# Performance work log

Measured on AMD Instinct MI355X. Metric: run time of the kernel, lower is better.

The kernel has to match this reference:

```python
import math
import jax, jax.numpy as jnp
import numpy as np

B, T, D = 128, 243, 1024   # batch, motion frames, latent_dim
N, L = 77, 512             # text tokens, text_latent_dim
H = 16                     # num_head -> head_dim 64
EPS = 1e-5


def _ln(x, g, b):
    m = x.mean(-1, keepdims=True)
    v = jnp.var(x, axis=-1, keepdims=True)
    return (x - m) * jax.lax.rsqrt(v + EPS) * g + b


def setup_inputs() -> dict:
    key = jax.random.key(0)
    ks = jax.random.split(key, 16)
    s = 0.02
    return {
        "x": jax.random.normal(ks[0], (B, T, D), jnp.float32),
        "xf": jax.random.normal(ks[1], (B, N, L), jnp.float32),
        "emb": jax.random.normal(ks[2], (B, T, D), jnp.float32),
        "ln_g": jnp.ones((D,), jnp.float32), "ln_b": jnp.zeros((D,), jnp.float32),
        "tln_g": jnp.ones((L,), jnp.float32), "tln_b": jnp.zeros((L,), jnp.float32),
        "Wq": jax.random.normal(ks[3], (D, D), jnp.float32) * s,
        "bq": jnp.zeros((D,), jnp.float32),
        "Wk": jax.random.normal(ks[4], (L, D), jnp.float32) * s,
        "bk": jnp.zeros((D,), jnp.float32),
        "Wv": jax.random.normal(ks[5], (L, D), jnp.float32) * s,
        "bv": jnp.zeros((D,), jnp.float32),
        "We": jax.random.normal(ks[6], (D, 2 * D), jnp.float32) * s,  # emb_layers Linear(time_embed_dim=D, 2D)
        "be": jnp.zeros((2 * D,), jnp.float32),
        "ln2_g": jnp.ones((D,), jnp.float32), "ln2_b": jnp.zeros((D,), jnp.float32),
        "Wo": jax.random.normal(ks[7], (D, D), jnp.float32) * s,     # zero_module in torch; random here for non-trivial baseline
        "bo": jnp.zeros((D,), jnp.float32),
    }


def reference(x, xf, emb, ln_g, ln_b, tln_g, tln_b, Wq, bq, Wk, bk, Wv, bv,
              We, be, ln2_g, ln2_b, Wo, bo):
    B_, T_, D_ = x.shape
    dh = D_ // H
    # cross-attention: queries from motion tokens, keys/values from text
    q = (_ln(x, ln_g, ln_b) @ Wq + bq).reshape(B_, T_, H, dh)
    xfn = _ln(xf, tln_g, tln_b)
    k = (xfn @ Wk + bk).reshape(B_, -1, H, dh)
    v = (xfn @ Wv + bv).reshape(B_, -1, H, dh)
    att = jnp.einsum('bthd,bnhd->btnh', q, k) / math.sqrt(dh)  # (B,T,N,H)
    w = jax.nn.softmax(att, axis=2)                            # softmax over text tokens; dropout is eval-mode identity
    y = jnp.einsum('btnh,bnhd->bthd', w, v).reshape(B_, T_, D_)
    # StylizationBlock (AdaLN): emb viewed (B,T,D), only first timestep used
    emb_out = (jax.nn.silu(emb) @ We + be)[:, 0:1, :]          # (B,1,2D)
    scale, shift = jnp.split(emb_out, 2, axis=2)
    h = _ln(y, ln2_g, ln2_b) * (1.0 + scale) + shift
    h = jax.nn.silu(h) @ Wo + bo
    return x + h
```

## Files before the change

kernel.cpp:

```cpp
#include <hip/hip_runtime.h>
#include <cstdint>

typedef __attribute__((ext_vector_type(8))) __bf16 bf16x8;
typedef __attribute__((ext_vector_type(4))) float f32x4;

__device__ __forceinline__ float b2f(unsigned short u) {
    union { uint32_t i; float f; } w; w.i = ((uint32_t)u) << 16; return w.f;
}
__device__ __forceinline__ unsigned short f2b(float f) {
    union { uint32_t i; float f; } w; w.f = f;
    uint32_t r = (w.i + 0x7FFFu + ((w.i >> 16) & 1u)) >> 16;
    return (unsigned short)r;
}

__device__ __forceinline__ void gl16(const unsigned short* g, unsigned short* l) {
    __builtin_amdgcn_global_load_lds(
        (const __attribute__((address_space(1))) void*)g,
        (__attribute__((address_space(3))) void*)l,
        16, 0, 0);
}

__global__ __launch_bounds__(256) void k_cvt(const float* __restrict__ in,
                                             unsigned short* __restrict__ out,
                                             int R, int C) {
    __shared__ float s[32][33];
    const int c0 = blockIdx.x * 32, r0 = blockIdx.y * 32;
    const int tx = threadIdx.x & 31, ty = threadIdx.x >> 5;
#pragma unroll
    for (int i = 0; i < 4; ++i)
        s[ty + i * 8][tx] = in[(size_t)(r0 + ty + i * 8) * C + c0 + tx];
    __syncthreads();
#pragma unroll
    for (int i = 0; i < 4; ++i)
        out[(size_t)(c0 + ty + i * 8) * R + r0 + tx] = f2b(s[tx][ty + i * 8]);
}

template <int DIM>
__global__ __launch_bounds__(256) void k_ln(const float* __restrict__ in,
                                            const float* __restrict__ g,
                                            const float* __restrict__ b,
                                            unsigned short* __restrict__ out) {
    const int row = blockIdx.x * 4 + (threadIdx.x >> 6);
    const int ln = threadIdx.x & 63;
    constexpr int PL = DIM / 64;
    float v[PL];
    const size_t base = (size_t)row * DIM + (size_t)ln * PL;
#pragma unroll
    for (int c = 0; c < PL; ++c) v[c] = in[base + c];
    float s = 0.f, s2 = 0.f;
#pragma unroll
    for (int c = 0; c < PL; ++c) { s += v[c]; s2 += v[c] * v[c]; }
    for (int o = 1; o < 64; o <<= 1) { s += __shfl_xor(s, o); s2 += __shfl_xor(s2, o); }
    const float mean = s / DIM;
    const float rstd = rsqrtf(s2 / DIM - mean * mean + 1e-5f);
#pragma unroll
    for (int c = 0; c < PL; ++c) {
        const int kk = ln * PL + c;
        out[(size_t)row * DIM + kk] = f2b((v[c] - mean) * rstd * g[kk] + b[kk]);
    }
}

__global__ __launch_bounds__(256) void k_silu(const float* __restrict__ emb,
                                              unsigned short* __restrict__ se) {
    const int i = blockIdx.x * 256 + threadIdx.x;
    const int b = i >> 10, k = i & 1023;
    const float f = emb[(size_t)b * (243 * 1024) + k];
    se[i] = f2b(f / (1.f + __expf(-f)));
}

template <int EPI>
__global__ __launch_bounds__(256, 2) void k_mm(
    const unsigned short* __restrict__ A, const unsigned short* __restrict__ Bt,
    const float* __restrict__ bias0, const float* __restrict__ bias1,
    unsigned short* __restrict__ C0, unsigned short* __restrict__ C1,
    float* __restrict__ Cf, const float* __restrict__ X,
    int N, int K) {
    __shared__ __align__(16) unsigned short sA[128 * 64];
    __shared__ __align__(16) unsigned short sB[128 * 64];
    const int tid = threadIdx.x, wv = tid >> 6, ln = tid & 63;
    const int wm = wv >> 1, wn = wv & 1;
    const int ln15 = ln & 15, lg = ln >> 4;

    const int NN = N >> 7;
    const int nwg = gridDim.x;
    const int wg = blockIdx.x;
    const int q = nwg >> 3, r = nwg & 7;
    const int xcd = wg & 7, idx = wg >> 3;
    const int u = (xcd < r) ? (xcd * (q + 1) + idx)
                            : (r * (q + 1) + (xcd - r) * q + idx);
    const int m0 = (u / NN) * 128, n0 = (u % NN) * 128;

    const f32x4 fz = {0.f, 0.f, 0.f, 0.f};
    f32x4 acc[4][4];
#pragma unroll
    for (int i = 0; i < 4; ++i)
#pragma unroll
        for (int j = 0; j < 4; ++j) acc[i][j] = fz;

    const int lrow = ln >> 3;
    const int sslot = (ln & 7) ^ lrow;
    const unsigned short* ga = A + (size_t)(m0 + wv * 32 + lrow) * K + sslot * 8;
    const unsigned short* gb = Bt + (size_t)(n0 + wv * 32 + lrow) * K + sslot * 8;
    unsigned short* const lA = sA + (wv * 32) * 64;
    unsigned short* const lB = sB + (wv * 32) * 64;

    for (int k0 = 0; k0 < K; k0 += 64) {
#pragma unroll
        for (int i = 0; i < 4; ++i) {
            gl16(ga + k0 + (size_t)i * 8 * K, lA + i * 8 * 64);
            gl16(gb + k0 + (size_t)i * 8 * K, lB + i * 8 * 64);
        }
        __syncthreads();
        bf16x8 af[4][2], bf[4][2];
#pragma unroll
        for (int i = 0; i < 4; ++i) {
            const int ra2 = wm * 64 + i * 16 + ln15;
            const int rb2 = wn * 64 + i * 16 + ln15;
#pragma unroll
            for (int ks = 0; ks < 2; ++ks) {
                const int slot = ks * 4 + lg;
                af[i][ks] = *(const bf16x8*)(sA + ra2 * 64 + ((slot ^ (ra2 & 7)) * 8));
                bf[i][ks] = *(const bf16x8*)(sB + rb2 * 64 + ((slot ^ (rb2 & 7)) * 8));
            }
        }
#pragma unroll
        for (int mi = 0; mi < 4; ++mi)
#pragma unroll
            for (int ni = 0; ni < 4; ++ni) {
                acc[mi][ni] = __builtin_amdgcn_mfma_f32_16x16x32_bf16(af[mi][0], bf[ni][0], acc[mi][ni], 0, 0, 0);
                acc[mi][ni] = __builtin_amdgcn_mfma_f32_16x16x32_bf16(af[mi][1], bf[ni][1], acc[mi][ni], 0, 0, 0);
            }
        __syncthreads();
    }

    const int colB = n0 + wn * 64;
    const int rowB = m0 + wm * 64;
#pragma unroll
    for (int mi = 0; mi < 4; ++mi) {
#pragma unroll
        for (int ni = 0; ni < 4; ++ni) {
            const int col = colB + ni * 16 + ln15;
            const int row = rowB + mi * 16 + lg * 4;
            float bvv;
            if (EPI == 2) bvv = (col < 1024) ? bias0[col] : bias1[col - 1024];
            else bvv = bias0[col];
#pragma unroll
            for (int r2 = 0; r2 < 4; ++r2) {
                const float v = acc[mi][ni][r2] + bvv;
                if (EPI == 0) {
                    C0[(size_t)(row + r2) * N + col] = f2b(v);
                } else if (EPI == 1) {
                    Cf[(size_t)(row + r2) * N + col] = v + X[(size_t)(row + r2) * N + col];
                } else if (EPI == 2) {
                    if (col < 1024) C0[(size_t)(row + r2) * 1024 + col] = f2b(v);
                    else C1[(size_t)(row + r2) * 1024 + (col - 1024)] = f2b(v);
                } else {
                    Cf[(size_t)(row + r2) * N + col] = v;
                }
            }
        }
    }
}

__global__ __launch_bounds__(256, 2) void k_attn_m(const unsigned short* __restrict__ Q,
                                                   const unsigned short* __restrict__ Kb,
                                                   const unsigned short* __restrict__ Vb,
                                                   unsigned short* __restrict__ Y) {
    __shared__ __align__(16) unsigned short sK[80 * 64];
    __shared__ __align__(16) unsigned short sV[64 * 96];
    __shared__ __align__(16) unsigned short sP[4][16 * 104];
    const int bh = blockIdx.x;
    const int b = bh >> 4, h = bh & 15;
    const int tid = threadIdx.x, wv = tid >> 6, ln = tid & 63;
    const int ln15 = ln & 15, lg = ln >> 4;

    for (int c = tid; c < 640; c += 256) {
        const int n = c >> 3, ci = c & 7;
        uint4 val = make_uint4(0u, 0u, 0u, 0u);
        if (n < 77) val = *(const uint4*)(Kb + (size_t)(b * 77 + n) * 1024 + h * 64 + ci * 8);
        *(uint4*)((char*)sK + n * 128 + ((ci * 16) ^ ((n & 7) << 4))) = val;
    }
    for (int i = tid; i < 64 * 96; i += 256) {
        const int d = i / 96, n = i - d * 96;
        unsigned short val = 0;
        if (n < 77) val = Vb[(size_t)(b * 77 + n) * 1024 + h * 64 + d];
        sV[i] = val;
    }
    for (int i = ln; i < 16 * 24; i += 64) {
        const int rr = i / 24, cc = i - rr * 24;
        sP[wv][rr * 104 + 80 + cc] = 0;
    }
    bf16x8 qf[4][2];
    const size_t qbase = (size_t)b * (243 * 1024) + h * 64;
#pragma unroll
    for (int mi = 0; mi < 4; ++mi) {
        int t = wv * 64 + mi * 16 + ln15;
        if (t > 242) t = 242;
#pragma unroll
        for (int ks = 0; ks < 2; ++ks)
            qf[mi][ks] = *(const bf16x8*)(Q + qbase + (size_t)t * 1024 + ks * 32 + lg * 8);
    }
    __syncthreads();

    const f32x4 fz = {0.f, 0.f, 0.f, 0.f};
    f32x4 yacc[4][4];
#pragma unroll
    for (int i = 0; i < 4; ++i)
#pragma unroll
        for (int j = 0; j < 4; ++j) yacc[i][j] = fz;

#pragma unroll
    for (int mi = 0; mi < 4; ++mi) {
        f32x4 sc[5];
#pragma unroll
        for (int ci = 0; ci < 5; ++ci) sc[ci] = fz;
#pragma unroll
        for (int ci = 0; ci < 5; ++ci) {
            const int n = ci * 16 + ln15;
#pragma unroll
            for (int ks = 0; ks < 2; ++ks) {
                const int kk = ks * 32 + lg * 8;
                bf16x8 kf = *(const bf16x8*)((const char*)sK + n * 128 + ((kk * 2) ^ ((n & 7) << 4)));
                sc[ci] = __builtin_amdgcn_mfma_f32_16x16x32_bf16(qf[mi][ks], kf, sc[ci], 0, 0, 0);
            }
        }
#pragma unroll
        for (int r = 0; r < 4; ++r) {
            float e[5];
            float mx = -1e30f;
#pragma unroll
            for (int ci = 0; ci < 5; ++ci) {
                const int n = ci * 16 + ln15;
                const float vv = (n < 77) ? sc[ci][r] * 0.125f : -1e30f;
                e[ci] = vv;
                mx = fmaxf(mx, vv);
            }
            mx = fmaxf(mx, __shfl_xor(mx, 1));
            mx = fmaxf(mx, __shfl_xor(mx, 2));
            mx = fmaxf(mx, __shfl_xor(mx, 4));
            mx = fmaxf(mx, __shfl_xor(mx, 8));
            float ssum = 0.f;
#pragma unroll
            for (int ci = 0; ci < 5; ++ci) {
                const int n = ci * 16 + ln15;
                const float ev = (n < 77) ? __expf(e[ci] - mx) : 0.f;
                e[ci] = ev;
                ssum += ev;
            }
            ssum += __shfl_xor(ssum, 1);
            ssum += __shfl_xor(ssum, 2);
            ssum += __shfl_xor(ssum, 4);
            ssum += __shfl_xor(ssum, 8);
            const float inv = 1.f / ssum;
            const int prow = lg * 4 + r;
#pragma unroll
            for (int ci = 0; ci < 5; ++ci)
                sP[wv][prow * 104 + ci * 16 + ln15] = f2b(e[ci] * inv);
        }
        __syncthreads();
#pragma unroll
        for (int ks = 0; ks < 3; ++ks) {
            bf16x8 pa = *(const bf16x8*)(sP[wv] + ln15 * 104 + ks * 32 + lg * 8);
#pragma unroll
            for (int di = 0; di < 4; ++di) {
                bf16x8 vf = *(const bf16x8*)(sV + (di * 16 + ln15) * 96 + ks * 32 + lg * 8);
                yacc[mi][di] = __builtin_amdgcn_mfma_f32_16x16x32_bf16(pa, vf, yacc[mi][di], 0, 0, 0);
            }
        }
        __syncthreads();
    }
    const size_t ybase = (size_t)b * (243 * 1024) + h * 64;
#pragma unroll
    for (int mi = 0; mi < 4; ++mi)
#pragma unroll
        for (int di = 0; di < 4; ++di)
#pragma unroll
            for (int r = 0; r < 4; ++r) {
                const int t = wv * 64 + mi * 16 + lg * 4 + r;
                if (t < 243) Y[ybase + (size_t)t * 1024 + di * 16 + ln15] = f2b(yacc[mi][di][r]);
            }
}

__global__ __launch_bounds__(256) void k_act(const unsigned short* __restrict__ y,
                                             const float* __restrict__ eo,
                                             const float* __restrict__ g,
                                             const float* __restrict__ b,
                                             unsigned short* __restrict__ out) {
    const int row = blockIdx.x * 4 + (threadIdx.x >> 6);
    const int ln = threadIdx.x & 63;
    const int bb = row / 243;
    float v[16];
    const size_t base = (size_t)row * 1024 + ln * 16;
#pragma unroll
    for (int c = 0; c < 16; ++c) v[c] = b2f(y[base + c]);
    float s = 0.f, s2 = 0.f;
#pragma unroll
    for (int c = 0; c < 16; ++c) { s += v[c]; s2 += v[c] * v[c]; }
    for (int o = 1; o < 64; o <<= 1) { s += __shfl_xor(s, o); s2 += __shfl_xor(s2, o); }
    const float mean = s / 1024.f;
    const float rstd = rsqrtf(s2 / 1024.f - mean * mean + 1e-5f);
#pragma unroll
    for (int c = 0; c < 16; ++c) {
        const int kk = ln * 16 + c;
        const float nl = (v[c] - mean) * rstd * g[kk] + b[kk];
        const float hh = nl * (1.f + eo[(size_t)bb * 2048 + kk]) + eo[(size_t)bb * 2048 + 1024 + kk];
        out[base + c] = f2b(hh / (1.f + __expf(-hh)));
    }
}

extern "C" void kernel_launch(void* const* d_in, const int* in_sizes, int n_in,
                              void* d_out, int out_size, void* d_ws, size_t ws_size,
                              hipStream_t stream) {
    (void)in_sizes; (void)n_in; (void)out_size; (void)ws_size;

    const float* x     = (const float*)d_in[0];
    const float* xf    = (const float*)d_in[1];
    const float* emb   = (const float*)d_in[2];
    const float* ln_g  = (const float*)d_in[3];
    const float* ln_b  = (const float*)d_in[4];
    const float* tln_g = (const float*)d_in[5];
    const float* tln_b = (const float*)d_in[6];
    const float* Wq    = (const float*)d_in[7];
    const float* bq    = (const float*)d_in[8];
    const float* Wk    = (const float*)d_in[9];
    const float* bk    = (const float*)d_in[10];
    const float* Wv    = (const float*)d_in[11];
    const float* bv    = (const float*)d_in[12];
    const float* We    = (const float*)d_in[13];
    const float* be    = (const float*)d_in[14];
    const float* ln2_g = (const float*)d_in[15];
    const float* ln2_b = (const float*)d_in[16];
    const float* Wo    = (const float*)d_in[17];
    const float* bo    = (const float*)d_in[18];
    float* outp = (float*)d_out;

    char* ws = (char*)d_ws;
    constexpr size_t o_wq   = 0;
    constexpr size_t o_wkv  = o_wq + 2097152;
    constexpr size_t o_we   = o_wkv + 2097152;
    constexpr size_t o_wo   = o_we + 4194304;
    constexpr size_t o_se   = o_wo + 2097152;
    constexpr size_t o_eo   = o_se + 262144;
    constexpr size_t o_xn   = o_eo + 1048576;
    constexpr size_t o_qb   = o_xn + 63700992;
    constexpr size_t o_xfn  = o_qb + 63700992;
    constexpr size_t o_kb   = o_xfn + 10092544;
    constexpr size_t o_vb   = o_kb + 20185088;

    unsigned short* wqt  = (unsigned short*)(ws + o_wq);
    unsigned short* wkvt = (unsigned short*)(ws + o_wkv);
    unsigned short* wet  = (unsigned short*)(ws + o_we);
    unsigned short* wot  = (unsigned short*)(ws + o_wo);
    unsigned short* se   = (unsigned short*)(ws + o_se);
    float*          eo   = (float*)(ws + o_eo);
    unsigned short* xn   = (unsigned short*)(ws + o_xn);
    unsigned short* yb   = xn;
    unsigned short* qb   = (unsigned short*)(ws + o_qb);
    unsigned short* actb = qb;
    unsigned short* xfn  = (unsigned short*)(ws + o_xfn);
    unsigned short* kb   = (unsigned short*)(ws + o_kb);
    unsigned short* vb   = (unsigned short*)(ws + o_vb);

    k_ln<1024><<<7776, 256, 0, stream>>>(x, ln_g, ln_b, xn);
    k_ln<512><<<2464, 256, 0, stream>>>(xf, tln_g, tln_b, xfn);
    k_silu<<<512, 256, 0, stream>>>(emb, se);
    k_cvt<<<dim3(32, 32), 256, 0, stream>>>(Wq, wqt, 1024, 1024);
    k_cvt<<<dim3(32, 16), 256, 0, stream>>>(Wk, wkvt, 512, 1024);
    k_cvt<<<dim3(32, 16), 256, 0, stream>>>(Wv, wkvt + 1024 * 512, 512, 1024);
    k_cvt<<<dim3(64, 32), 256, 0, stream>>>(We, wet, 1024, 2048);
    k_cvt<<<dim3(32, 32), 256, 0, stream>>>(Wo, wot, 1024, 1024);

    k_mm<3><<<16, 256, 0, stream>>>(se, wet, be, nullptr,
                                    nullptr, nullptr, eo, nullptr, 2048, 1024);

    k_mm<0><<<243 * 8, 256, 0, stream>>>(xn, wqt, bq, nullptr,
                                         qb, nullptr, nullptr, nullptr, 1024, 1024);
    k_mm<2><<<77 * 16, 256, 0, stream>>>(xfn, wkvt, bk, bv,
                                         kb, vb, nullptr, nullptr, 2048, 512);

    k_attn_m<<<2048, 256, 0, stream>>>(qb, kb, vb, yb);

    k_act<<<7776, 256, 0, stream>>>(yb, eo, ln2_g, ln2_b, actb);

    k_mm<1><<<243 * 8, 256, 0, stream>>>(actb, wot, bo, nullptr,
                                         nullptr, nullptr, outp, x, 1024, 1024);
}
```

Measured before the change: 397.3 us.

## Merge weight conversions into one launch, vectorize LN/act I/O, drop attention syncs

The five weight transpose-convert launches become a single kernel that picks its matrix from the block index, cutting launch overhead. The LayerNorm and activation kernels now load and store through float4 and 8-wide bf16 vectors instead of scalar accesses, aiming for better memory coalescing. The two __syncthreads around the per-wave P buffer in the attention loop are removed because each wave uses its own sP slice. Removing the trailing sync risks a hazard on shared K/V tiles reloaded in the next iteration if the loop refills them.

```diff
diff --git a/kernel.cpp b/kernel.cpp
--- a/kernel.cpp
+++ b/kernel.cpp
@@ -3,6 +3,7 @@
 
 typedef __attribute__((ext_vector_type(8))) __bf16 bf16x8;
 typedef __attribute__((ext_vector_type(4))) float f32x4;
+typedef __attribute__((ext_vector_type(8))) unsigned short ushort8v;
 
 __device__ __forceinline__ float b2f(unsigned short u) {
     union { uint32_t i; float f; } w; w.i = ((uint32_t)u) << 16; return w.f;
@@ -20,11 +21,22 @@
         16, 0, 0);
 }
 
-__global__ __launch_bounds__(256) void k_cvt(const float* __restrict__ in,
-                                             unsigned short* __restrict__ out,
-                                             int R, int C) {
+__global__ __launch_bounds__(256) void k_cvt_all(
+    const float* __restrict__ Wq, const float* __restrict__ Wk,
+    const float* __restrict__ Wv, const float* __restrict__ We,
+    const float* __restrict__ Wo,
+    unsigned short* __restrict__ wqt, unsigned short* __restrict__ wkvt,
+    unsigned short* __restrict__ wet, unsigned short* __restrict__ wot) {
     __shared__ float s[32][33];
-    const int c0 = blockIdx.x * 32, r0 = blockIdx.y * 32;
+    int bid = blockIdx.x;
+    const float* in; unsigned short* out; int R, C;
+    if (bid < 1024)      { in = Wq; out = wqt;              R = 1024; C = 1024; }
+    else if (bid < 1536) { bid -= 1024; in = Wk; out = wkvt;             R = 512;  C = 1024; }
+    else if (bid < 2048) { bid -= 1536; in = Wv; out = wkvt + 1024 * 512; R = 512;  C = 1024; }
+    else if (bid < 4096) { bid -= 2048; in = We; out = wet;              R = 1024; C = 2048; }
+    else                 { bid -= 4096; in = Wo; out = wot;              R = 1024; C = 1024; }
+    const int ctiles = C >> 5;
+    const int c0 = (bid % ctiles) * 32, r0 = (bid / ctiles) * 32;
     const int tx = threadIdx.x & 31, ty = threadIdx.x >> 5;
 #pragma unroll
     for (int i = 0; i < 4; ++i)
@@ -45,18 +57,31 @@
     constexpr int PL = DIM / 64;
     float v[PL];
     const size_t base = (size_t)row * DIM + (size_t)ln * PL;
-#pragma unroll
-    for (int c = 0; c < PL; ++c) v[c] = in[base + c];
+    const float4* p4 = (const float4*)(in + base);
+#pragma unroll
+    for (int c = 0; c < PL / 4; ++c) {
+        const float4 t = p4[c];
+        v[c * 4 + 0] = t.x; v[c * 4 + 1] = t.y; v[c * 4 + 2] = t.z; v[c * 4 + 3] = t.w;
+    }
     float s = 0.f, s2 = 0.f;
 #pragma unroll
     for (int c = 0; c < PL; ++c) { s += v[c]; s2 += v[c] * v[c]; }
     for (int o = 1; o < 64; o <<= 1) { s += __shfl_xor(s, o); s2 += __shfl_xor(s2, o); }
     const float mean = s / DIM;
     const float rstd = rsqrtf(s2 / DIM - mean * mean + 1e-5f);
-#pragma unroll
-    for (int c = 0; c < PL; ++c) {
-        const int kk = ln * PL + c;
-        out[(size_t)row * DIM + kk] = f2b((v[c] - mean) * rstd * g[kk] + b[kk]);
+    const float4* g4 = (const float4*)(g + ln * PL);
+    const float4* b4 = (const float4*)(b + ln * PL);
+#pragma unroll
+    for (int c0 = 0; c0 < PL; c0 += 8) {
+        ushort8v yv;
+#pragma unroll
+        for (int j = 0; j < 8; ++j) {
+            const int c = c0 + j;
+            const float gg = ((const float*)g4)[c];
+            const float bb = ((const float*)b4)[c];
+            yv[j] = f2b((v[c] - mean) * rstd * gg + bb);
+        }
+        *(ushort8v*)(out + base + c0) = yv;
     }
 }
 
@@ -257,7 +282,6 @@
             for (int ci = 0; ci < 5; ++ci)
                 sP[wv][prow * 104 + ci * 16 + ln15] = f2b(e[ci] * inv);
         }
-        __syncthreads();
 #pragma unroll
         for (int ks = 0; ks < 3; ++ks) {
             bf16x8 pa = *(const bf16x8*)(sP[wv] + ln15 * 104 + ks * 32 + lg * 8);
@@ -267,7 +291,6 @@
                 yacc[mi][di] = __builtin_amdgcn_mfma_f32_16x16x32_bf16(pa, vf, yacc[mi][di], 0, 0, 0);
             }
         }
-        __syncthreads();
     }
     const size_t ybase = (size_t)b * (243 * 1024) + h * 64;
 #pragma unroll
@@ -292,19 +315,32 @@
     float v[16];
     const size_t base = (size_t)row * 1024 + ln * 16;
 #pragma unroll
-    for (int c = 0; c < 16; ++c) v[c] = b2f(y[base + c]);
+    for (int c0 = 0; c0 < 16; c0 += 8) {
+        const ushort8v t = *(const ushort8v*)(y + base + c0);
+#pragma unroll
+        for (int j = 0; j < 8; ++j) v[c0 + j] = b2f(t[j]);
+    }
     float s = 0.f, s2 = 0.f;
 #pragma unroll
     for (int c = 0; c < 16; ++c) { s += v[c]; s2 += v[c] * v[c]; }
     for (int o = 1; o < 64; o <<= 1) { s += __shfl_xor(s, o); s2 += __shfl_xor(s2, o); }
     const float mean = s / 1024.f;
     const float rstd = rsqrtf(s2 / 1024.f - mean * mean + 1e-5f);
-#pragma unroll
-    for (int c = 0; c < 16; ++c) {
-        const int kk = ln * 16 + c;
-        const float nl = (v[c] - mean) * rstd * g[kk] + b[kk];
-        const float hh = nl * (1.f + eo[(size_t)bb * 2048 + kk]) + eo[(size_t)bb * 2048 + 1024 + kk];
-        out[base + c] = f2b(hh / (1.f + __expf(-hh)));
+    const float* gp = g + ln * 16;
+    const float* bp = b + ln * 16;
+    const float* sc = eo + (size_t)bb * 2048 + ln * 16;
+    const float* sh = sc + 1024;
+#pragma unroll
+    for (int c0 = 0; c0 < 16; c0 += 8) {
+        ushort8v yv;
+#pragma unroll
+        for (int j = 0; j < 8; ++j) {
+            const int c = c0 + j;
+            const float nl = (v[c] - mean) * rstd * gp[c] + bp[c];
+            const float hh = nl * (1.f + sc[c]) + sh[c];
+            yv[j] = f2b(hh / (1.f + __expf(-hh)));
+        }
+        *(ushort8v*)(out + base + c0) = yv;
     }
 }
 
@@ -364,11 +400,7 @@
     k_ln<1024><<<7776, 256, 0, stream>>>(x, ln_g, ln_b, xn);
     k_ln<512><<<2464, 256, 0, stream>>>(xf, tln_g, tln_b, xfn);
     k_silu<<<512, 256, 0, stream>>>(emb, se);
-    k_cvt<<<dim3(32, 32), 256, 0, stream>>>(Wq, wqt, 1024, 1024);
-    k_cvt<<<dim3(32, 16), 256, 0, stream>>>(Wk, wkvt, 512, 1024);
-    k_cvt<<<dim3(32, 16), 256, 0, stream>>>(Wv, wkvt + 1024 * 512, 512, 1024);
-    k_cvt<<<dim3(64, 32), 256, 0, stream>>>(We, wet, 1024, 2048);
-    k_cvt<<<dim3(32, 32), 256, 0, stream>>>(Wo, wot, 1024, 1024);
+    k_cvt_all<<<5120, 256, 0, stream>>>(Wq, Wk, Wv, We, Wo, wqt, wkvt, wet, wot);
 
     k_mm<3><<<16, 256, 0, stream>>>(se, wet, be, nullptr,
                                     nullptr, nullptr, eo, nullptr, 2048, 1024);
```

Measured after the change: 392.6 us. About the same (-1.2%).
